# Optimization experiments

Hardware: AMD Instinct MI355X
Metric: run time of the kernel (lower is better)

Reference implementation:

```python
import jax, jax.numpy as jnp
import numpy as np

N_HEADS = 8
FACTOR = 5
N_LAYERS = 2
D_MODEL = 512


def _pos_enc(L, d):
    pos = jnp.arange(L, dtype=jnp.float32)[:, None]
    div = jnp.exp(jnp.arange(0, d, 2, dtype=jnp.float32) * (-np.log(10000.0) / d))
    pe = jnp.zeros((L, d), dtype=jnp.float32)
    pe = pe.at[:, 0::2].set(jnp.sin(pos * div))
    pe = pe.at[:, 1::2].set(jnp.cos(pos * div))
    return pe


def _ln(x, g, b, eps=1e-5):
    mu = x.mean(-1, keepdims=True)
    var = ((x - mu) ** 2).mean(-1, keepdims=True)
    return (x - mu) * jax.lax.rsqrt(var + eps) * g + b


def _token_conv(x, W):
    # x: [B, L, C_in]; W: [d_model, C_in, 3]; circular padding k=3 (Informer TokenEmbedding)
    xt = jnp.transpose(x, (0, 2, 1))
    xt = jnp.concatenate([xt[:, :, -1:], xt, xt[:, :, :1]], axis=-1)
    y = jax.lax.conv_general_dilated(xt, W, (1,), 'VALID', dimension_numbers=('NCH', 'OIH', 'NCH'))
    return jnp.transpose(y, (0, 2, 1))


def _prob_attention(Q, K, V):
    # ProbSparse attention (Informer). Q,K,V: [B,H,L,D]
    B, H, L, D = Q.shape
    ln_L = int(np.ceil(np.log(L)))
    U_part = min(FACTOR * ln_L, L)  # sampled keys per query
    u = min(FACTOR * ln_L, L)       # top queries kept
    idx = jax.random.randint(jax.random.key(42), (L, U_part), 0, L)  # shared across B,H as in torch
    K_sample = K[:, :, idx, :]                                  # [B,H,L,U_part,D]
    QK_sample = jnp.einsum('bhld,bhlud->bhlu', Q, K_sample)
    M = QK_sample.max(-1) - QK_sample.mean(-1)                  # sparsity measure [B,H,L]
    _, M_top = jax.lax.top_k(M, u)                              # [B,H,u]
    Q_reduce = jnp.take_along_axis(Q, M_top[..., None], axis=2) # [B,H,u,D]
    scores = jnp.einsum('bhud,bhld->bhul', Q_reduce, K) / jnp.sqrt(jnp.float32(D))
    attn = jax.nn.softmax(scores, axis=-1)
    ctx = jnp.broadcast_to(V.mean(axis=2, keepdims=True), Q.shape)  # non-selected -> mean(V)
    upd = jnp.einsum('bhul,bhld->bhud', attn, V)
    bi = jnp.arange(B)[:, None, None]
    hi = jnp.arange(H)[None, :, None]
    return ctx.at[bi, hi, M_top].set(upd)                       # scatter selected queries


def reference(x_state_enc, x_enc, x_mark_enc, state_emb_W, token_conv_W, time_W, time_b,
              Wq, bq, Wk, bk, Wv, bv, Wo, bo, ln1_g, ln1_b, ln2_g, ln2_b,
              ffn1_W, ffn1_b, ffn2_W, ffn2_b, norm_g, norm_b):
    B, L = x_state_enc.shape
    dm = D_MODEL
    H = N_HEADS
    dk = dm // H
    # StatePosEmbedding: state emb + token conv emb + time-feature linear + sinusoidal pos
    x = state_emb_W[x_state_enc] + _token_conv(x_enc, token_conv_W) + x_mark_enc @ time_W + time_b + _pos_enc(L, dm)
    for l in range(N_LAYERS):
        q = (x @ Wq[l] + bq[l]).reshape(B, L, H, dk).transpose(0, 2, 1, 3)
        k = (x @ Wk[l] + bk[l]).reshape(B, L, H, dk).transpose(0, 2, 1, 3)
        v = (x @ Wv[l] + bv[l]).reshape(B, L, H, dk).transpose(0, 2, 1, 3)
        ctx = _prob_attention(q, k, v).transpose(0, 2, 1, 3).reshape(B, L, dm)
        x = x + (ctx @ Wo[l] + bo[l])
        x = _ln(x, ln1_g[l], ln1_b[l])
        y = jax.nn.gelu(x @ ffn1_W[l] + ffn1_b[l], approximate=False)
        y = y @ ffn2_W[l] + ffn2_b[l]
        x = _ln(x + y, ln2_g[l], ln2_b[l])
    x = _ln(x, norm_g, norm_b)
    logits = x[:, -1:, :] @ state_emb_W.T  # pred_len = 1
    return logits[:, :, :-1]


def setup_inputs() -> dict:
    key = jax.random.key(0)
    ks = jax.random.split(key, 16)
    B, L, C_IN, MARK = 4, 2048, 7, 4
    NG = 100
    dm, dff, NL = 512, 2048, 2
    s = 0.02
    return {
        'x_state_enc': jax.random.randint(ks[0], (B, L), 0, NG + 1),
        'x_enc': jax.random.normal(ks[1], (B, L, C_IN), dtype=jnp.float32),
        'x_mark_enc': jax.random.normal(ks[2], (B, L, MARK), dtype=jnp.float32),
        'state_emb_W': jax.random.normal(ks[3], (NG + 1, dm), dtype=jnp.float32) * s,
        'token_conv_W': jax.random.normal(ks[4], (dm, C_IN, 3), dtype=jnp.float32) * s,
        'time_W': jax.random.normal(ks[5], (MARK, dm), dtype=jnp.float32) * s,
        'time_b': jnp.zeros((dm,), jnp.float32),
        'Wq': jax.random.normal(ks[6], (NL, dm, dm), dtype=jnp.float32) * s,
        'bq': jnp.zeros((NL, dm), jnp.float32),
        'Wk': jax.random.normal(ks[7], (NL, dm, dm), dtype=jnp.float32) * s,
        'bk': jnp.zeros((NL, dm), jnp.float32),
        'Wv': jax.random.normal(ks[8], (NL, dm, dm), dtype=jnp.float32) * s,
        'bv': jnp.zeros((NL, dm), jnp.float32),
        'Wo': jax.random.normal(ks[9], (NL, dm, dm), dtype=jnp.float32) * s,
        'bo': jnp.zeros((NL, dm), jnp.float32),
        'ln1_g': jnp.ones((NL, dm), jnp.float32),
        'ln1_b': jnp.zeros((NL, dm), jnp.float32),
        'ln2_g': jnp.ones((NL, dm), jnp.float32),
        'ln2_b': jnp.zeros((NL, dm), jnp.float32),
        'ffn1_W': jax.random.normal(ks[10], (NL, dm, dff), dtype=jnp.float32) * s,
        'ffn1_b': jnp.zeros((NL, dff), jnp.float32),
        'ffn2_W': jax.random.normal(ks[11], (NL, dff, dm), dtype=jnp.float32) * s,
        'ffn2_b': jnp.zeros((NL, dm), jnp.float32),
        'norm_g': jnp.ones((dm,), jnp.float32),
        'norm_b': jnp.zeros((dm,), jnp.float32),
    }
```

## Files before the change

kernel.cpp:

```cpp
#include <hip/hip_runtime.h>
#include <hip/hip_bf16.h>

#define L_SEQ 2048
#define NB    4
#define DM    512
#define NH    8
#define DK    64
#define DFF   2048
#define NSAMP 40
#define NGRID 100
#define PARTC 16
#define CKEY  128

typedef __attribute__((ext_vector_type(8))) short bf16x8;
typedef __attribute__((ext_vector_type(4))) float f32x4;

__device__ __forceinline__ unsigned rotl32(unsigned x, unsigned r){ return (x<<r)|(x>>(32u-r)); }
__device__ __forceinline__ float bf2f(ushort u){ return __uint_as_float(((unsigned)u)<<16); }
__device__ __forceinline__ ushort f2bf(float f){
  unsigned u = __float_as_uint(f);
  unsigned r = (u + 0x7fffu + ((u>>16)&1u)) >> 16;
  return (ushort)r;
}

__device__ __forceinline__ void threefry2x32(unsigned k0, unsigned k1, unsigned x0, unsigned x1,
                                             unsigned &o0, unsigned &o1){
  unsigned ks0=k0, ks1=k1, ks2=k0^k1^0x1BD11BDAu;
  x0 += ks0; x1 += ks1;
#define RND(r) { x0 += x1; x1 = rotl32(x1, r); x1 ^= x0; }
  RND(13u) RND(15u) RND(26u) RND(6u)   x0+=ks1; x1+=ks2+1u;
  RND(17u) RND(29u) RND(16u) RND(24u)  x0+=ks2; x1+=ks0+2u;
  RND(13u) RND(15u) RND(26u) RND(6u)   x0+=ks0; x1+=ks1+3u;
  RND(17u) RND(29u) RND(16u) RND(24u)  x0+=ks1; x1+=ks2+4u;
  RND(13u) RND(15u) RND(26u) RND(6u)   x0+=ks2; x1+=ks0+5u;
#undef RND
  o0=x0; o1=x1;
}

__global__ __launch_bounds__(256) void k_prep(
    const float* __restrict__ Wq, const float* __restrict__ Wk,
    const float* __restrict__ Wv, const float* __restrict__ Wo,
    const float* __restrict__ f1W, const float* __restrict__ f2W,
    const float* __restrict__ bq, const float* __restrict__ bk, const float* __restrict__ bv,
    ushort* __restrict__ wt, float* __restrict__ bcat, int* __restrict__ sidx)
{
  const size_t F1T=1048576, F2T=2097152, LSTR=3145728;
  int bid = blockIdx.x, t = threadIdx.x;
  if (bid >= 6145){
    int i = (bid-6145)*256 + t;
    const int total = L_SEQ*NSAMP;
    if (i < total){
      unsigned o0, o1;
      threefry2x32(0u, 42u, 0u, (unsigned)(total + i), o0, o1);
      sidx[i] = (int)((o0 ^ o1) & (unsigned)(L_SEQ-1));
    }
    return;
  }
  if (bid == 6144){
    for (int i=t; i<2*1536; i+=256){
      int l = i / 1536, r = i - l*1536;
      float v = (r<512) ? bq[l*DM+r] : (r<1024) ? bk[l*DM+r-512] : bv[l*DM+r-1024];
      bcat[i] = v;
    }
    return;
  }
  int l = bid >= 3072; bid -= l*3072;
  const float* src; ushort* dst; int K, N, tile;
  if (bid < 1024){
    int m = bid >> 8; tile = bid & 255;
    src = (m==0?Wq:m==1?Wk:m==2?Wv:Wo) + (size_t)l*DM*DM;
    dst = wt + (size_t)l*LSTR + (size_t)m*262144; K=DM; N=DM;
  } else if (bid < 2048){
    tile = bid-1024; src = f1W + (size_t)l*DM*DFF; dst = wt + (size_t)l*LSTR + F1T; K=DM; N=DFF;
  } else {
    tile = bid-2048; src = f2W + (size_t)l*DFF*DM; dst = wt + (size_t)l*LSTR + F2T; K=DFF; N=DM;
  }
  int ntn = N/32;
  int n0 = (tile % ntn)*32, k0 = (tile / ntn)*32;
  __shared__ float tl[32][33];
  int r = t >> 5, c = t & 31;
  for (int rr=r; rr<32; rr+=8) tl[rr][c] = src[(size_t)(k0+rr)*N + n0 + c];
  __syncthreads();
  for (int rr=r; rr<32; rr+=8)
    dst[(size_t)(n0+rr)*K + k0 + c] = f2bf(tl[c][rr]);
}

__global__ __launch_bounds__(256) void k_embed(const int* __restrict__ tok,
    const float* __restrict__ x_enc, const float* __restrict__ x_mark,
    const float* __restrict__ embW, const float* __restrict__ convW,
    const float* __restrict__ timeW, const float* __restrict__ timeb,
    float* __restrict__ x, ushort* __restrict__ xb){
  int bl = blockIdx.x; int b = bl >> 11; int l = bl & (L_SEQ-1);
  __shared__ float xin[21];
  __shared__ float xm[4];
  int t = threadIdx.x;
  if (t < 21){
    int tt = t/7, i = t - tt*7;
    int ll = (l + tt - 1) & (L_SEQ-1);
    xin[t] = x_enc[((size_t)b*L_SEQ + ll)*7 + i];
  }
  if (t >= 32 && t < 36) xm[t-32] = x_mark[((size_t)b*L_SEQ + l)*4 + (t-32)];
  __syncthreads();
  int tk = tok[bl];
  #pragma unroll
  for (int rep=0; rep<2; rep++){
    int d = t + rep*256;
    float v = embW[(size_t)tk*DM + d];
    const float* w = convW + (size_t)d*21;
    float cv = 0.f;
    #pragma unroll
    for (int tt=0; tt<3; tt++)
      #pragma unroll
      for (int i=0; i<7; i++)
        cv = fmaf(xin[tt*7+i], w[i*3+tt], cv);
    v += cv;
    float tv = timeb[d];
    #pragma unroll
    for (int m=0; m<4; m++) tv = fmaf(xm[m], timeW[m*DM + d], tv);
    v += tv;
    int j = d >> 1;
    float div = expf((float)(2*j) * (-0.017988946039015984f));
    float ang = (float)l * div;
    v += (d & 1) ? cosf(ang) : sinf(ang);
    x[(size_t)bl*DM + d] = v;
    xb[(size_t)bl*DM + d] = f2bf(v);
  }
}

enum { MG_ADD=0, MG_GELU_BF16=1, MG_QKV=2 };

__global__ __launch_bounds__(256) void k_mgemm(
    const ushort* __restrict__ A, const ushort* __restrict__ Bt,
    const float* __restrict__ bias, float* __restrict__ Cf,
    ushort* __restrict__ Cb, int M, int N, int K, int mode)
{
  __shared__ ushort As[64][64];
  __shared__ ushort Bs[64][64];
  int tid = threadIdx.x, lane = tid & 63, wid = tid >> 6;
  int m0 = blockIdx.y*64, n0 = blockIdx.x*64;
  int wr = wid >> 1, wc = wid & 1;
  f32x4 acc[2][2];
  #pragma unroll
  for (int i=0;i<2;i++)
    #pragma unroll
    for(int j=0;j<2;j++) acc[i][j] = (f32x4){0.f,0.f,0.f,0.f};

  for (int k0 = 0; k0 < K; k0 += 64){
    __syncthreads();
    #pragma unroll
    for (int it=0; it<2; it++){
      int e   = it*256 + tid;
      int row = e >> 3, seg = e & 7;
      __builtin_amdgcn_global_load_lds(
        (const __attribute__((address_space(1))) void*)(A + (size_t)(m0+row)*K + k0 + seg*8),
        (__attribute__((address_space(3))) void*)(&As[0][0] + (size_t)e*8), 16, 0, 0);
      __builtin_amdgcn_global_load_lds(
        (const __attribute__((address_space(1))) void*)(Bt + (size_t)(n0+row)*K + k0 + seg*8),
        (__attribute__((address_space(3))) void*)(&Bs[0][0] + (size_t)e*8), 16, 0, 0);
    }
    __syncthreads();
    #pragma unroll
    for (int kk=0; kk<2; kk++){
      bf16x8 af[2], bfv[2];
      int ko = kk*32 + (lane>>4)*8;
      #pragma unroll
      for (int i=0;i<2;i++) af[i]  = *(const bf16x8*)&As[wr*32 + i*16 + (lane&15)][ko];
      #pragma unroll
      for (int j=0;j<2;j++) bfv[j] = *(const bf16x8*)&Bs[wc*32 + j*16 + (lane&15)][ko];
      #pragma unroll
      for (int i=0;i<2;i++)
        #pragma unroll
        for (int j=0;j<2;j++)
          acc[i][j] = __builtin_amdgcn_mfma_f32_16x16x32_bf16(af[i], bfv[j], acc[i][j], 0,0,0);
    }
  }

  int fq = lane >> 4, fr = lane & 15;
  for (int i=0;i<2;i++){
    for (int j=0;j<2;j++){
      #pragma unroll
      for (int jj=0;jj<4;jj++){
        int r = m0 + wr*32 + i*16 + fq*4 + jj;
        int c = n0 + wc*32 + j*16 + fr;
        float v = acc[i][j][jj] + bias[c];
        if (mode == MG_ADD){
          Cf[(size_t)r*N + c] += v;
        } else if (mode == MG_GELU_BF16){
          float g = 0.5f*v*(1.f + erff(v*0.70710678118654752f));
          Cb[(size_t)r*N + c] = f2bf(g);
        } else {
          int b = r >> 11, l = r & (L_SEQ-1), m3 = c >> 9, hh = (c>>6)&7, d = c & 63;
          Cb[(size_t)m3*4194304 + (((size_t)b*NH + hh)*L_SEQ + l)*64 + d] = f2bf(v);
        }
      }
    }
  }
}

__global__ __launch_bounds__(256) void k_vmean1(const ushort* __restrict__ V, float* __restrict__ part){
  int blk = blockIdx.x;
  int bh = blk >> 5, ch = blk & 31;
  int t = threadIdx.x, d = t & 63, c = t >> 6;
  const ushort* Vb = V + (size_t)bh*L_SEQ*DK + (size_t)(ch*64 + c*16)*DK;
  float s = 0.f;
  #pragma unroll
  for (int r=0; r<16; r++) s += bf2f(Vb[r*DK + d]);
  __shared__ float red[256];
  red[t]=s; __syncthreads();
  if (t < 64) part[(size_t)blk*64 + t] = red[t]+red[t+64]+red[t+128]+red[t+192];
}
__global__ __launch_bounds__(64) void k_vmean2(const float* __restrict__ part, float* __restrict__ vmean){
  int bh = blockIdx.x, d = threadIdx.x;
  float s = 0.f;
  #pragma unroll
  for (int ch=0; ch<32; ch++) s += part[(size_t)(bh*32+ch)*64 + d];
  vmean[bh*64+d] = s * (1.f/(float)L_SEQ);
}

__global__ __launch_bounds__(256) void k_mscore(const ushort* __restrict__ Q, const ushort* __restrict__ Km,
    const int* __restrict__ idx, float* __restrict__ M){
  int wid = threadIdx.x >> 6, lane = threadIdx.x & 63;
  int g = blockIdx.x*4 + wid;
  int l = g & (L_SEQ-1), bh = g >> 11;
  __shared__ float qs[4][64];
  qs[wid][lane] = bf2f(Q[(size_t)g*64 + lane]);
  __syncthreads();
  float dot = 0.f;
  if (lane < NSAMP){
    const ushort* kr = Km + (size_t)bh*L_SEQ*64 + (size_t)idx[l*NSAMP+lane]*64;
    #pragma unroll
    for (int c8=0; c8<8; c8++){
      bf16x8 kv = *(const bf16x8*)(kr + c8*8);
      #pragma unroll
      for (int jj=0; jj<8; jj++) dot = fmaf(qs[wid][c8*8+jj], bf2f((ushort)kv[jj]), dot);
    }
  }
  float mx = (lane < NSAMP) ? dot : -INFINITY;
  float sm = (lane < NSAMP) ? dot : 0.f;
  for (int off=32; off; off>>=1){
    mx = fmaxf(mx, __shfl_xor(mx, off));
    sm += __shfl_xor(sm, off);
  }
  if (lane==0) M[g] = mx - sm*(1.f/(float)NSAMP);
}

__global__ __launch_bounds__(64) void k_topk(const float* __restrict__ M, int* __restrict__ Mtop){
  int bh = blockIdx.x, lane = threadIdx.x;
  float v[32];
  #pragma unroll
  for (int s=0; s<32; s++) v[s] = M[(size_t)bh*L_SEQ + s*64 + lane];
  for (int sel=0; sel<NSAMP; sel++){
    float best = -INFINITY; int bs = 0;
    #pragma unroll
    for (int s=0; s<32; s++){
      if (v[s] > best){ best = v[s]; bs = s; }
    }
    int bidx = bs*64 + lane;
    #pragma unroll
    for (int off=1; off<64; off<<=1){
      float ov = __shfl_xor(best, off);
      int   oi = __shfl_xor(bidx, off);
      if (ov > best || (ov == best && oi < bidx)){ best = ov; bidx = oi; }
    }
    if (lane == 0) Mtop[bh*NSAMP + sel] = bidx;
    int cs = bidx >> 6, cl = bidx & 63;
    if (lane == cl){
      #pragma unroll
      for (int s=0; s<32; s++) if (s == cs) v[s] = -INFINITY;
    }
  }
}

__global__ __launch_bounds__(256) void k_ctxfill(const float* __restrict__ vmean, ushort* __restrict__ ctx){
  int i = blockIdx.x*256 + threadIdx.x;
  int c = i & (DM-1);
  int b = i >> 20;
  int h = c >> 6, d = c & 63;
  ctx[i] = f2bf(vmean[((b<<3)+h)*64 + d]);
}

__global__ __launch_bounds__(256) void k_attn1(const ushort* __restrict__ Q, const ushort* __restrict__ K,
    const ushort* __restrict__ V, const int* __restrict__ Mtop,
    float* __restrict__ pm, float* __restrict__ ps, float* __restrict__ pO){
  int bid = blockIdx.x;
  int xcd = bid & 7, idx = bid >> 3;
  int bh = xcd*4 + (idx & 3), ch = idx >> 2;
  int l0 = ch * CKEY;
  int t = threadIdx.x, lane = t & 63, w = t >> 6;

  __shared__ ushort Qs[48][64];
  __shared__ ushort Ks[CKEY][64];
  __shared__ ushort Vs[CKEY][66];
  __shared__ ushort Ps[48][136];
  __shared__ float rmax[4][48];
  __shared__ float rsum[4][48];
  __shared__ float Oacc[48][64];
  __shared__ int qidx[48];

  if (t < 40) qidx[t] = Mtop[bh*NSAMP + t];
  const ushort* Kb = K + ((size_t)bh*L_SEQ + l0)*64;
  #pragma unroll
  for (int i=0;i<4;i++){
    int e = i*256 + t;
    __builtin_amdgcn_global_load_lds(
      (const __attribute__((address_space(1))) void*)(Kb + (size_t)e*8),
      (__attribute__((address_space(3))) void*)(&Ks[0][0] + (size_t)e*8), 16, 0, 0);
  }
  __syncthreads();

  const ushort* Qb = Q + (size_t)bh*L_SEQ*64;
  {
    int row = t >> 3, seg = t & 7;
    bf16x8 qv = *(const bf16x8*)(Qb + (size_t)qidx[row]*64 + seg*8);
    *(bf16x8*)&Qs[row][seg*8] = qv;
    if (t < 128){
      int r2 = 32 + (t>>3);
      bf16x8 z = (bf16x8){0,0,0,0,0,0,0,0};
      if (r2 < 40) z = *(const bf16x8*)(Qb + (size_t)qidx[r2]*64 + (t&7)*8);
      *(bf16x8*)&Qs[r2][(t&7)*8] = z;
    }
  }
  const ushort* Vb = V + ((size_t)bh*L_SEQ + l0)*64;
  #pragma unroll
  for (int i=0;i<4;i++){
    int e = i*256 + t;
    int row = e >> 3, seg = e & 7;
    bf16x8 vv = *(const bf16x8*)(Vb + (size_t)e*8);
    *(bf16x8*)&Vs[row][seg*8] = vv;
  }
  __syncthreads();

  for (int i=t; i<48*64; i+=256) ((float*)Oacc)[i] = 0.f;

  f32x4 sa[3][2];
  #pragma unroll
  for (int i=0;i<3;i++) for (int j=0;j<2;j++) sa[i][j] = (f32x4){0.f,0.f,0.f,0.f};
  #pragma unroll
  for (int ks=0; ks<2; ks++){
    int ko = ks*32 + (lane>>4)*8;
    bf16x8 af[3], bf[2];
    #pragma unroll
    for (int i=0;i<3;i++) af[i] = *(const bf16x8*)&Qs[i*16 + (lane&15)][ko];
    #pragma unroll
    for (int j=0;j<2;j++) bf[j] = *(const bf16x8*)&Ks[w*32 + j*16 + (lane&15)][ko];
    #pragma unroll
    for (int i=0;i<3;i++)
      #pragma unroll
      for (int j=0;j<2;j++)
        sa[i][j] = __builtin_amdgcn_mfma_f32_16x16x32_bf16(af[i], bf[j], sa[i][j], 0,0,0);
  }
  #pragma unroll
  for (int i=0;i<3;i++)
    #pragma unroll
    for (int j=0;j<2;j++)
      #pragma unroll
      for (int jj=0;jj<4;jj++) sa[i][j][jj] *= 0.125f;
  #pragma unroll
  for (int i=0;i<3;i++){
    #pragma unroll
    for (int jj=0;jj<4;jj++){
      float mx = fmaxf(sa[i][0][jj], sa[i][1][jj]);
      #pragma unroll
      for (int off=1; off<16; off<<=1) mx = fmaxf(mx, __shfl_xor(mx, off));
      if ((lane&15)==0) rmax[w][i*16 + (lane>>4)*4 + jj] = mx;
    }
  }
  __syncthreads();
  #pragma unroll
  for (int i=0;i<3;i++){
    #pragma unroll
    for (int jj=0;jj<4;jj++){
      int row = i*16 + (lane>>4)*4 + jj;
      float m = fmaxf(fmaxf(rmax[0][row], rmax[1][row]), fmaxf(rmax[2][row], rmax[3][row]));
      float p0 = __expf(sa[i][0][jj] - m);
      float p1 = __expf(sa[i][1][jj] - m);
      Ps[row][w*32 + (lane&15)]      = f2bf(p0);
      Ps[row][w*32 + 16 + (lane&15)] = f2bf(p1);
      float sm = p0 + p1;
      #pragma unroll
      for (int off=1; off<16; off<<=1) sm += __shfl_xor(sm, off);
      if ((lane&15)==0) rsum[w][row] = sm;
    }
  }
  __syncthreads();

  f32x4 oa[3][4];
  #pragma unroll
  for (int i=0;i<3;i++) for (int j=0;j<4;j++) oa[i][j] = (f32x4){0.f,0.f,0.f,0.f};
  {
    bf16x8 pa[3], vb[4];
    int kbase = w*32 + (lane>>4)*8;
    #pragma unroll
    for (int i=0;i<3;i++) pa[i] = *(const bf16x8*)&Ps[i*16 + (lane&15)][kbase];
    #pragma unroll
    for (int j=0;j<4;j++){
      #pragma unroll
      for (int e=0;e<8;e++) vb[j][e] = (short)Vs[kbase + e][j*16 + (lane&15)];
    }
    #pragma unroll
    for (int i=0;i<3;i++)
      #pragma unroll
      for (int j=0;j<4;j++)
        oa[i][j] = __builtin_amdgcn_mfma_f32_16x16x32_bf16(pa[i], vb[j], oa[i][j], 0,0,0);
  }
  #pragma unroll
  for (int ww=0; ww<4; ww++){
    if (w == ww){
      #pragma unroll
      for (int i=0;i<3;i++)
        #pragma unroll
        for (int j=0;j<4;j++)
          #pragma unroll
          for (int jj=0;jj<4;jj++)
            Oacc[i*16 + (lane>>4)*4 + jj][j*16 + (lane&15)] += oa[i][j][jj];
    }
    __syncthreads();
  }

  size_t base = ((size_t)bh*PARTC + ch);
  if (t < 40){
    float m = fmaxf(fmaxf(rmax[0][t], rmax[1][t]), fmaxf(rmax[2][t], rmax[3][t]));
    pm[base*40 + t] = m;
    ps[base*40 + t] = rsum[0][t]+rsum[1][t]+rsum[2][t]+rsum[3][t];
  }
  {
    int row = t >> 3, d0 = (t&7)*8;
    float* dst = pO + (base*48 + row)*64 + d0;
    #pragma unroll
    for (int e=0;e<8;e++) dst[e] = Oacc[row][d0+e];
    if (t < 64){
      int r2 = 32 + (t>>3);
      float* dst2 = pO + (base*48 + r2)*64 + d0;
      #pragma unroll
      for (int e=0;e<8;e++) dst2[e] = Oacc[r2][d0+e];
    }
  }
}

__global__ __launch_bounds__(256) void k_attn2(const float* __restrict__ pm, const float* __restrict__ ps,
    const float* __restrict__ pO, const int* __restrict__ Mtop, ushort* __restrict__ ctx){
  int bh = blockIdx.x, b = bh >> 3, h = bh & 7;
  int t = threadIdx.x;
  __shared__ float wch[PARTC][40];
  __shared__ float inv_s[40];
  __shared__ int qidx[40];
  if (t < 40){
    qidx[t] = Mtop[bh*NSAMP + t];
    float m = -INFINITY;
    #pragma unroll
    for (int c=0;c<PARTC;c++) m = fmaxf(m, pm[((size_t)bh*PARTC + c)*40 + t]);
    float s = 0.f;
    #pragma unroll
    for (int c=0;c<PARTC;c++){
      float wc = __expf(pm[((size_t)bh*PARTC + c)*40 + t] - m);
      wch[c][t] = wc;
      s += wc * ps[((size_t)bh*PARTC + c)*40 + t];
    }
    inv_s[t] = 1.f / s;
  }
  __syncthreads();
  #pragma unroll
  for (int iter=0; iter<2; iter++){
    int row = iter*32 + (t>>3);
    if (row < 40){
      int d0 = (t&7)*8;
      float o[8] = {0.f,0.f,0.f,0.f,0.f,0.f,0.f,0.f};
      for (int c=0;c<PARTC;c++){
        const float* pp = pO + (((size_t)bh*PARTC + c)*48 + row)*64 + d0;
        float wc = wch[c][row];
        float4 a = *(const float4*)pp, b4 = *(const float4*)(pp+4);
        o[0]=fmaf(wc,a.x,o[0]); o[1]=fmaf(wc,a.y,o[1]); o[2]=fmaf(wc,a.z,o[2]); o[3]=fmaf(wc,a.w,o[3]);
        o[4]=fmaf(wc,b4.x,o[4]); o[5]=fmaf(wc,b4.y,o[5]); o[6]=fmaf(wc,b4.z,o[6]); o[7]=fmaf(wc,b4.w,o[7]);
      }
      float is = inv_s[row];
      bf16x8 wv;
      #pragma unroll
      for (int e=0;e<8;e++) wv[e] = (short)f2bf(o[e]*is);
      *(bf16x8*)(ctx + ((size_t)b*L_SEQ + qidx[row])*DM + h*64 + d0) = wv;
    }
  }
}

__global__ __launch_bounds__(256) void k_ln(float* __restrict__ x,
    const float* __restrict__ g, const float* __restrict__ b,
    ushort* __restrict__ xb){
  int row = blockIdx.x*4 + (threadIdx.x>>6);
  int lane = threadIdx.x & 63;
  float* xr = x + (size_t)row*DM + lane*8;
  float4 v0 = *(const float4*)(xr);
  float4 v1 = *(const float4*)(xr + 4);
  float s = v0.x+v0.y+v0.z+v0.w+v1.x+v1.y+v1.z+v1.w;
  #pragma unroll
  for (int off=1; off<64; off<<=1) s += __shfl_xor(s, off);
  float mu = s * (1.f/(float)DM);
  float d0=v0.x-mu, d1=v0.y-mu, d2=v0.z-mu, d3=v0.w-mu;
  float d4=v1.x-mu, d5=v1.y-mu, d6=v1.z-mu, d7=v1.w-mu;
  float q = d0*d0+d1*d1+d2*d2+d3*d3+d4*d4+d5*d5+d6*d6+d7*d7;
  #pragma unroll
  for (int off=1; off<64; off<<=1) q += __shfl_xor(q, off);
  float r = rsqrtf(q * (1.f/(float)DM) + 1e-5f);
  float4 g0 = *(const float4*)(g + lane*8);
  float4 g1 = *(const float4*)(g + lane*8 + 4);
  float4 b0 = *(const float4*)(b + lane*8);
  float4 b1 = *(const float4*)(b + lane*8 + 4);
  float o0=d0*r*g0.x+b0.x, o1=d1*r*g0.y+b0.y, o2=d2*r*g0.z+b0.z, o3=d3*r*g0.w+b0.w;
  float o4=d4*r*g1.x+b1.x, o5=d5*r*g1.y+b1.y, o6=d6*r*g1.z+b1.z, o7=d7*r*g1.w+b1.w;
  *(float4*)(xr)     = (float4){o0,o1,o2,o3};
  *(float4*)(xr + 4) = (float4){o4,o5,o6,o7};
  if (xb){
    bf16x8 w;
    w[0]=(short)f2bf(o0); w[1]=(short)f2bf(o1); w[2]=(short)f2bf(o2); w[3]=(short)f2bf(o3);
    w[4]=(short)f2bf(o4); w[5]=(short)f2bf(o5); w[6]=(short)f2bf(o6); w[7]=(short)f2bf(o7);
    *(bf16x8*)(xb + (size_t)row*DM + lane*8) = w;
  }
}

__global__ __launch_bounds__(64) void k_logits(const float* __restrict__ x, const float* __restrict__ embW,
                                               float* __restrict__ out){
  int bid = blockIdx.x;
  int b = bid / NGRID, g = bid - b*NGRID;
  const float* xr = x + ((size_t)b*L_SEQ + (L_SEQ-1))*DM;
  const float* er = embW + (size_t)g*DM;
  int lane = threadIdx.x;
  float s = 0.f;
  for (int d=lane; d<DM; d+=64) s = fmaf(xr[d], er[d], s);
  for (int off=32; off; off>>=1) s += __shfl_xor(s, off);
  if (lane==0) out[bid] = s;
}

extern "C" void kernel_launch(void* const* d_in, const int* in_sizes, int n_in,
                              void* d_out, int out_size, void* d_ws, size_t ws_size,
                              hipStream_t stream) {
  const int*   tok    = (const int*)d_in[0];
  const float* x_enc  = (const float*)d_in[1];
  const float* x_mark = (const float*)d_in[2];
  const float* embW   = (const float*)d_in[3];
  const float* convW  = (const float*)d_in[4];
  const float* timeW  = (const float*)d_in[5];
  const float* timeb  = (const float*)d_in[6];
  const float* Wq = (const float*)d_in[7];  const float* bq = (const float*)d_in[8];
  const float* Wk = (const float*)d_in[9];  const float* bk = (const float*)d_in[10];
  const float* Wv = (const float*)d_in[11]; const float* bv = (const float*)d_in[12];
  const float* Wo = (const float*)d_in[13]; const float* bo = (const float*)d_in[14];
  const float* ln1g = (const float*)d_in[15]; const float* ln1b = (const float*)d_in[16];
  const float* ln2g = (const float*)d_in[17]; const float* ln2b = (const float*)d_in[18];
  const float* f1W = (const float*)d_in[19]; const float* f1b = (const float*)d_in[20];
  const float* f2W = (const float*)d_in[21]; const float* f2b = (const float*)d_in[22];
  const float* nrmg = (const float*)d_in[23]; const float* nrmb = (const float*)d_in[24];
  float* out = (float*)d_out;

  char* ws = (char*)d_ws;
  float*  x    = (float*) (ws);
  ushort* xb   = (ushort*)(ws + ((size_t)16<<20));
  ushort* q    = (ushort*)(ws + ((size_t)24<<20));
  ushort* kbuf = (ushort*)(ws + ((size_t)32<<20));
  ushort* vbuf = (ushort*)(ws + ((size_t)40<<20));
  ushort* ctx  = (ushort*)(ws + ((size_t)48<<20));
  ushort* hbuf = (ushort*)(ws + ((size_t)24<<20));
  ushort* wt   = (ushort*)(ws + ((size_t)56<<20));
  float*  Mbuf = (float*) (ws + ((size_t)69<<20));
  int*    Mtop = (int*)   (ws + ((size_t)70<<20));
  int*    sidx = (int*)   (ws + ((size_t)71<<20));
  float*  vmean= (float*) (ws + ((size_t)72<<20));
  float*  bcat = (float*) (ws + ((size_t)73<<20));
  float*  part = (float*) (ws + ((size_t)74<<20));
  float*  pO   = (float*) (ws + ((size_t)75<<20));
  float*  pmb  = (float*) (ws + ((size_t)82<<20));
  float*  psb  = (float*) (ws + ((size_t)82<<20) + 102400);

  const int Mrows = NB*L_SEQ;
  const size_t WQT=0, WOT=786432, F1T=1048576, F2T=2097152, LSTR=3145728;

  k_prep<<<6465, 256, 0, stream>>>(Wq, Wk, Wv, Wo, f1W, f2W, bq, bk, bv, wt, bcat, sidx);
  k_embed<<<NB*L_SEQ, 256, 0, stream>>>(tok, x_enc, x_mark, embW, convW, timeW, timeb, x, xb);

  for (int l=0; l<2; l++){
    size_t b5 = (size_t)l*DM;
    ushort* wl = wt + (size_t)l*LSTR;

    k_mgemm<<<dim3(1536/64, Mrows/64), 256, 0, stream>>>(xb, wl+WQT, bcat+l*1536, nullptr, q, Mrows, 1536, DM, MG_QKV);
    k_vmean1<<<NB*NH*32, 256, 0, stream>>>(vbuf, part);
    k_vmean2<<<NB*NH, 64, 0, stream>>>(part, vmean);
    k_mscore<<<NB*NH*L_SEQ/4, 256, 0, stream>>>(q, kbuf, sidx, Mbuf);
    k_topk<<<NB*NH, 64, 0, stream>>>(Mbuf, Mtop);
    k_ctxfill<<<(NB*L_SEQ*DM)/256, 256, 0, stream>>>(vmean, ctx);
    k_attn1<<<NB*NH*PARTC, 256, 0, stream>>>(q, kbuf, vbuf, Mtop, pmb, psb, pO);
    k_attn2<<<NB*NH, 256, 0, stream>>>(pmb, psb, pO, Mtop, ctx);
    k_mgemm<<<dim3(DM/64, Mrows/64), 256, 0, stream>>>(ctx, wl+WOT, bo+b5, x, nullptr, Mrows, DM, DM, MG_ADD);
    k_ln<<<Mrows/4, 256, 0, stream>>>(x, ln1g+b5, ln1b+b5, xb);
    k_mgemm<<<dim3(DFF/64, Mrows/64), 256, 0, stream>>>(xb, wl+F1T, f1b + (size_t)l*DFF, nullptr, hbuf, Mrows, DFF, DM, MG_GELU_BF16);
    k_mgemm<<<dim3(DM/64, Mrows/64), 256, 0, stream>>>(hbuf, wl+F2T, f2b+b5, x, nullptr, Mrows, DM, DFF, MG_ADD);
    k_ln<<<Mrows/4, 256, 0, stream>>>(x, ln2g+b5, ln2b+b5, xb);
  }
  k_ln<<<Mrows/4, 256, 0, stream>>>(x, nrmg, nrmb, nullptr);
  k_logits<<<NB*NGRID, 64, 0, stream>>>(x, embW, out);
}
```

Baseline: 604.7 us.

## Enlarge GEMM tiles to 128x128 and parallelize sparsity score across lanes

The bf16 MFMA GEMM block tile grows from 64x64 to 128x128, with each wave computing 4x4 fragments, to increase operand reuse and cut LDS traffic per FLOP. Launch grids are adjusted to match. The ProbSparse score kernel now splits each sampled-key dot product across 8 lanes with vectorized loads and shuffle reductions, so all 64 lanes are busy. The larger tiles reduce block counts for the narrow N=512 GEMMs, which may leave the GPU underfilled and raise register pressure.

```diff
diff --git a/kernel.cpp b/kernel.cpp
--- a/kernel.cpp
+++ b/kernel.cpp
@@ -134,54 +134,57 @@
     const float* __restrict__ bias, float* __restrict__ Cf,
     ushort* __restrict__ Cb, int M, int N, int K, int mode)
 {
-  __shared__ ushort As[64][64];
-  __shared__ ushort Bs[64][64];
+  __shared__ ushort As[128][64];
+  __shared__ ushort Bs[128][64];
   int tid = threadIdx.x, lane = tid & 63, wid = tid >> 6;
-  int m0 = blockIdx.y*64, n0 = blockIdx.x*64;
+  int m0 = blockIdx.y*128, n0 = blockIdx.x*128;
   int wr = wid >> 1, wc = wid & 1;
-  f32x4 acc[2][2];
-  #pragma unroll
-  for (int i=0;i<2;i++)
-    #pragma unroll
-    for(int j=0;j<2;j++) acc[i][j] = (f32x4){0.f,0.f,0.f,0.f};
+  f32x4 acc[4][4];
+  #pragma unroll
+  for (int i=0;i<4;i++)
+    #pragma unroll
+    for(int j=0;j<4;j++) acc[i][j] = (f32x4){0.f,0.f,0.f,0.f};
+
+  int lrow = lane >> 3;
+  int lcol = (lane & 7) * 8;
 
   for (int k0 = 0; k0 < K; k0 += 64){
     __syncthreads();
     #pragma unroll
-    for (int it=0; it<2; it++){
-      int e   = it*256 + tid;
-      int row = e >> 3, seg = e & 7;
+    for (int t=0; t<4; t++){
+      int inst = wid*4 + t;
+      int row = inst*8 + lrow;
       __builtin_amdgcn_global_load_lds(
-        (const __attribute__((address_space(1))) void*)(A + (size_t)(m0+row)*K + k0 + seg*8),
-        (__attribute__((address_space(3))) void*)(&As[0][0] + (size_t)e*8), 16, 0, 0);
+        (const __attribute__((address_space(1))) void*)(A + (size_t)(m0+row)*K + k0 + lcol),
+        (__attribute__((address_space(3))) void*)(&As[inst*8][0]), 16, 0, 0);
       __builtin_amdgcn_global_load_lds(
-        (const __attribute__((address_space(1))) void*)(Bt + (size_t)(n0+row)*K + k0 + seg*8),
-        (__attribute__((address_space(3))) void*)(&Bs[0][0] + (size_t)e*8), 16, 0, 0);
+        (const __attribute__((address_space(1))) void*)(Bt + (size_t)(n0+row)*K + k0 + lcol),
+        (__attribute__((address_space(3))) void*)(&Bs[inst*8][0]), 16, 0, 0);
     }
     __syncthreads();
     #pragma unroll
     for (int kk=0; kk<2; kk++){
-      bf16x8 af[2], bfv[2];
+      bf16x8 af[4], bfv[4];
       int ko = kk*32 + (lane>>4)*8;
       #pragma unroll
-      for (int i=0;i<2;i++) af[i]  = *(const bf16x8*)&As[wr*32 + i*16 + (lane&15)][ko];
-      #pragma unroll
-      for (int j=0;j<2;j++) bfv[j] = *(const bf16x8*)&Bs[wc*32 + j*16 + (lane&15)][ko];
-      #pragma unroll
-      for (int i=0;i<2;i++)
+      for (int i=0;i<4;i++) af[i]  = *(const bf16x8*)&As[wr*64 + i*16 + (lane&15)][ko];
+      #pragma unroll
+      for (int j=0;j<4;j++) bfv[j] = *(const bf16x8*)&Bs[wc*64 + j*16 + (lane&15)][ko];
+      #pragma unroll
+      for (int i=0;i<4;i++)
         #pragma unroll
-        for (int j=0;j<2;j++)
+        for (int j=0;j<4;j++)
           acc[i][j] = __builtin_amdgcn_mfma_f32_16x16x32_bf16(af[i], bfv[j], acc[i][j], 0,0,0);
     }
   }
 
   int fq = lane >> 4, fr = lane & 15;
-  for (int i=0;i<2;i++){
-    for (int j=0;j<2;j++){
+  for (int i=0;i<4;i++){
+    for (int j=0;j<4;j++){
       #pragma unroll
       for (int jj=0;jj<4;jj++){
-        int r = m0 + wr*32 + i*16 + fq*4 + jj;
-        int c = n0 + wc*32 + j*16 + fr;
+        int r = m0 + wr*64 + i*16 + fq*4 + jj;
+        int c = n0 + wc*64 + j*16 + fr;
         float v = acc[i][j][jj] + bias[c];
         if (mode == MG_ADD){
           Cf[(size_t)r*N + c] += v;
@@ -222,26 +225,39 @@
   int wid = threadIdx.x >> 6, lane = threadIdx.x & 63;
   int g = blockIdx.x*4 + wid;
   int l = g & (L_SEQ-1), bh = g >> 11;
-  __shared__ float qs[4][64];
-  qs[wid][lane] = bf2f(Q[(size_t)g*64 + lane]);
-  __syncthreads();
-  float dot = 0.f;
-  if (lane < NSAMP){
-    const ushort* kr = Km + (size_t)bh*L_SEQ*64 + (size_t)idx[l*NSAMP+lane]*64;
-    #pragma unroll
-    for (int c8=0; c8<8; c8++){
-      bf16x8 kv = *(const bf16x8*)(kr + c8*8);
-      #pragma unroll
-      for (int jj=0; jj<8; jj++) dot = fmaf(qs[wid][c8*8+jj], bf2f((ushort)kv[jj]), dot);
-    }
-  }
-  float mx = (lane < NSAMP) ? dot : -INFINITY;
-  float sm = (lane < NSAMP) ? dot : 0.f;
-  for (int off=32; off; off>>=1){
+  int sg = lane >> 3, dg = lane & 7;
+
+  bf16x8 qv = *(const bf16x8*)(Q + (size_t)g*64 + dg*8);
+  float qf[8];
+  #pragma unroll
+  for (int e=0;e<8;e++) qf[e] = bf2f((ushort)qv[e]);
+
+  const int* ir = idx + l*NSAMP;
+  int ki[5];
+  #pragma unroll
+  for (int i=0;i<5;i++) ki[i] = ir[i*8 + sg];
+  const ushort* Kb = Km + (size_t)bh*L_SEQ*64;
+  bf16x8 kv[5];
+  #pragma unroll
+  for (int i=0;i<5;i++) kv[i] = *(const bf16x8*)(Kb + (size_t)ki[i]*64 + dg*8);
+
+  float mx = -INFINITY, sm = 0.f;
+  #pragma unroll
+  for (int i=0;i<5;i++){
+    float d = 0.f;
+    #pragma unroll
+    for (int e=0;e<8;e++) d = fmaf(qf[e], bf2f((ushort)kv[i][e]), d);
+    #pragma unroll
+    for (int off=1; off<8; off<<=1) d += __shfl_xor(d, off);
+    mx = fmaxf(mx, d);
+    sm += d;
+  }
+  #pragma unroll
+  for (int off=1; off<64; off<<=1){
     mx = fmaxf(mx, __shfl_xor(mx, off));
     sm += __shfl_xor(sm, off);
   }
-  if (lane==0) M[g] = mx - sm*(1.f/(float)NSAMP);
+  if (lane==0) M[g] = mx - sm * (1.f/(8.f*(float)NSAMP));
 }
 
 __global__ __launch_bounds__(64) void k_topk(const float* __restrict__ M, int* __restrict__ Mtop){
@@ -578,7 +594,7 @@
     size_t b5 = (size_t)l*DM;
     ushort* wl = wt + (size_t)l*LSTR;
 
-    k_mgemm<<<dim3(1536/64, Mrows/64), 256, 0, stream>>>(xb, wl+WQT, bcat+l*1536, nullptr, q, Mrows, 1536, DM, MG_QKV);
+    k_mgemm<<<dim3(1536/128, Mrows/128), 256, 0, stream>>>(xb, wl+WQT, bcat+l*1536, nullptr, q, Mrows, 1536, DM, MG_QKV);
     k_vmean1<<<NB*NH*32, 256, 0, stream>>>(vbuf, part);
     k_vmean2<<<NB*NH, 64, 0, stream>>>(part, vmean);
     k_mscore<<<NB*NH*L_SEQ/4, 256, 0, stream>>>(q, kbuf, sidx, Mbuf);
@@ -586,10 +602,10 @@
     k_ctxfill<<<(NB*L_SEQ*DM)/256, 256, 0, stream>>>(vmean, ctx);
     k_attn1<<<NB*NH*PARTC, 256, 0, stream>>>(q, kbuf, vbuf, Mtop, pmb, psb, pO);
     k_attn2<<<NB*NH, 256, 0, stream>>>(pmb, psb, pO, Mtop, ctx);
-    k_mgemm<<<dim3(DM/64, Mrows/64), 256, 0, stream>>>(ctx, wl+WOT, bo+b5, x, nullptr, Mrows, DM, DM, MG_ADD);
+    k_mgemm<<<dim3(DM/128, Mrows/128), 256, 0, stream>>>(ctx, wl+WOT, bo+b5, x, nullptr, Mrows, DM, DM, MG_ADD);
     k_ln<<<Mrows/4, 256, 0, stream>>>(x, ln1g+b5, ln1b+b5, xb);
-    k_mgemm<<<dim3(DFF/64, Mrows/64), 256, 0, stream>>>(xb, wl+F1T, f1b + (size_t)l*DFF, nullptr, hbuf, Mrows, DFF, DM, MG_GELU_BF16);
-    k_mgemm<<<dim3(DM/64, Mrows/64), 256, 0, stream>>>(hbuf, wl+F2T, f2b+b5, x, nullptr, Mrows, DM, DFF, MG_ADD);
+    k_mgemm<<<dim3(DFF/128, Mrows/128), 256, 0, stream>>>(xb, wl+F1T, f1b + (size_t)l*DFF, nullptr, hbuf, Mrows, DFF, DM, MG_GELU_BF16);
+    k_mgemm<<<dim3(DM/128, Mrows/128), 256, 0, stream>>>(hbuf, wl+F2T, f2b+b5, x, nullptr, Mrows, DM, DFF, MG_ADD);
     k_ln<<<Mrows/4, 256, 0, stream>>>(x, ln2g+b5, ln2b+b5, xb);
   }
   k_ln<<<Mrows/4, 256, 0, stream>>>(x, nrmg, nrmb, nullptr);
```

Result: slower. 1.048 ms (+73.2%).
